# Performance work log

Measured on AMD Instinct MI355X. Metric: run time of the kernel, lower is better.

## Reference

```python
import jax, jax.numpy as jnp
import numpy as np

N = 50000
E = 400000
T = 7
FEAT = 7
H = 64
OUT = 4
LN_EPS = 1e-5


def _w(key, shape, scale=0.1):
    return jax.random.normal(key, shape, jnp.float32) * scale


def setup_inputs() -> dict:
    key = jax.random.key(0)
    ks = list(jax.random.split(key, 16))
    p = {}
    p['x'] = jax.random.normal(ks[0], (N, T, FEAT), jnp.float32)
    p['edge_index'] = jax.random.randint(ks[1], (2, E), 0, N)
    p['edge_weight'] = jax.random.uniform(ks[2], (E,), jnp.float32)
    p['Wg1'] = _w(ks[3], (FEAT, H)); p['bg1'] = jnp.zeros((H,), jnp.float32)
    p['Wg2'] = _w(ks[4], (H, H));    p['bg2'] = jnp.zeros((H,), jnp.float32)
    p['ln_g'] = jnp.ones((H,), jnp.float32); p['ln_b'] = jnp.zeros((H,), jnp.float32)
    p['Wih0'] = _w(ks[5], (4 * H, H)); p['Whh0'] = _w(ks[6], (4 * H, H))
    p['bih0'] = jnp.zeros((4 * H,), jnp.float32); p['bhh0'] = jnp.zeros((4 * H,), jnp.float32)
    p['Wih1'] = _w(ks[7], (4 * H, H)); p['Whh1'] = _w(ks[8], (4 * H, H))
    p['bih1'] = jnp.zeros((4 * H,), jnp.float32); p['bhh1'] = jnp.zeros((4 * H,), jnp.float32)
    p['Wm1'] = _w(ks[9], (H, H // 2));  p['bm1'] = jnp.zeros((H // 2,), jnp.float32)
    p['Wm2'] = _w(ks[10], (H // 2, OUT)); p['bm2'] = jnp.zeros((OUT,), jnp.float32)
    p['Wd1'] = _w(ks[11], (H, H // 4)); p['bd1'] = jnp.zeros((H // 4,), jnp.float32)
    p['Wd2'] = _w(ks[12], (H // 4, OUT)); p['bd2'] = jnp.zeros((OUT,), jnp.float32)
    return p


def gcn_norm(edge_index, edge_weight, n):
    # PyG GCNConv default: add self-loops (weight 1), symmetric normalization
    loop = jnp.arange(n)
    src = jnp.concatenate([edge_index[0], loop])
    dst = jnp.concatenate([edge_index[1], loop])
    w = jnp.concatenate([edge_weight, jnp.ones((n,), edge_weight.dtype)])
    deg = jax.ops.segment_sum(w, dst, num_segments=n)
    dinv = jnp.where(deg > 0, jax.lax.rsqrt(deg), 0.0)
    return src, dst, dinv[src] * w * dinv[dst]


def gcn(h, W, b, src, dst, norm, n):
    h = h @ W                          # [N, H] linear transform first
    m = h[src] * norm[:, None]         # gather + edge scaling  [E', H]
    return jax.ops.segment_sum(m, dst, num_segments=n) + b


def layer_norm(h, g, b):
    mu = jnp.mean(h, -1, keepdims=True)
    v = jnp.mean((h - mu) ** 2, -1, keepdims=True)
    return (h - mu) * jax.lax.rsqrt(v + LN_EPS) * g + b


def lstm_layer(xs, Wih, Whh, bih, bhh):
    # xs: [N, T, H]; torch gate order i, f, g, o
    n = xs.shape[0]
    h0 = jnp.zeros((n, Whh.shape[1]), xs.dtype)
    def step(carry, xt):
        h, c = carry
        gates = xt @ Wih.T + h @ Whh.T + bih + bhh
        i, f, g, o = jnp.split(gates, 4, axis=-1)
        c = jax.nn.sigmoid(f) * c + jax.nn.sigmoid(i) * jnp.tanh(g)
        h = jax.nn.sigmoid(o) * jnp.tanh(c)
        return (h, c), h
    _, hs = jax.lax.scan(step, (h0, h0), jnp.swapaxes(xs, 0, 1))
    return jnp.swapaxes(hs, 0, 1)


def reference(x, edge_index, edge_weight, Wg1, bg1, Wg2, bg2, ln_g, ln_b,
              Wih0, Whh0, bih0, bhh0, Wih1, Whh1, bih1, bhh1,
              Wm1, bm1, Wm2, bm2, Wd1, bd1, Wd2, bd2):
    n = x.shape[0]
    src, dst, norm = gcn_norm(edge_index, edge_weight, n)
    outs = []
    for t in range(x.shape[1]):  # fixed small T=7 (lookback)
        h = gcn(x[:, t, :], Wg1, bg1, src, dst, norm, n)
        h = jax.nn.leaky_relu(h, 0.01)
        # dropout is identity in eval mode
        h = gcn(h, Wg2, bg2, src, dst, norm, n)
        h = jax.nn.leaky_relu(h, 0.01)
        h = layer_norm(h, ln_g, ln_b)
        outs.append(h)
    seq = jnp.stack(outs, axis=1)  # [N, T, H]
    seq = lstm_layer(seq, Wih0, Whh0, bih0, bhh0)
    seq = lstm_layer(seq, Wih1, Whh1, bih1, bhh1)
    f = seq[:, -1, :]
    magnitude = jax.nn.relu(jax.nn.leaky_relu(f @ Wm1 + bm1, 0.01) @ Wm2 + bm2) + 1e-4
    direction = jax.nn.relu(f @ Wd1 + bd1) @ Wd2 + bd2
    return (magnitude, direction)
```

## Files before the change

### kernel.cpp

```cpp
#include <hip/hip_runtime.h>
#include <stdint.h>

#define NN 50000
#define NP 50048
#define EE 400000
#define TT 7
#define LN_EPS 1e-5f
#define SIG_SC (-1.4426950408889634f)
#define TANH_SC (2.8853900817779268f)

typedef __attribute__((ext_vector_type(8))) short bf16x8;
typedef __attribute__((ext_vector_type(4))) float f32x4;

__device__ __forceinline__ float leaky01(float x){ return x > 0.f ? x : 0.01f*x; }
__device__ __forceinline__ float fastrcp(float x){ return __builtin_amdgcn_rcpf(x); }
__device__ __forceinline__ float exp2fast(float x){ return __builtin_amdgcn_exp2f(x); }
__device__ __forceinline__ float sigmoidf(float x){ return fastrcp(1.f+__expf(-x)); }
__device__ __forceinline__ float tanhfast(float x){ return 1.f - 2.f*fastrcp(__expf(2.f*x)+1.f); }
__device__ __forceinline__ unsigned bf16rne(float f){
  unsigned u = __float_as_uint(f);
  return (u + 0x7fffu + ((u>>16)&1u)) >> 16;
}
__device__ __forceinline__ float bfu(unsigned u){ return __uint_as_float(u<<16); }
__device__ __forceinline__ float bfhi(unsigned u){ return __uint_as_float(u & 0xffff0000u); }

__global__ __launch_bounds__(256) void k_prep_all(
    const float* __restrict__ Wih0, const float* __restrict__ Whh0,
    const float* __restrict__ Wih1, const float* __restrict__ Whh1,
    const float* __restrict__ Wg2,
    const float* __restrict__ bih0, const float* __restrict__ bhh0,
    const float* __restrict__ bih1, const float* __restrict__ bhh1,
    const float* __restrict__ x,
    uint4* __restrict__ WF, uint4* __restrict__ WG2F, float* __restrict__ BS,
    ushort* __restrict__ xb, float* __restrict__ deg, int* __restrict__ counts){
  int b = blockIdx.x, tid = threadIdx.x;
  if (b < 32){
    int idx = b*256 + tid;
    int L = idx >> 12;
    int r = idx & 4095;
    int lane = r & 63;
    int e = r >> 6;
    int which = e & 1;
    int cs = e >> 1;
    int s = cs & 1, ct = cs >> 1;
    int row = ct*16 + (lane & 15);
    float sc = ((row >> 6) == 2) ? TANH_SC : SIG_SC;
    int kb = s*32 + (lane >> 4)*8;
    const float* W = L ? (which ? Whh1 : Wih1) : (which ? Whh0 : Wih0);
    const float* p = W + row*64 + kb;
    uint4 v;
    v.x = bf16rne(sc*p[0]) | (bf16rne(sc*p[1])<<16);
    v.y = bf16rne(sc*p[2]) | (bf16rne(sc*p[3])<<16);
    v.z = bf16rne(sc*p[4]) | (bf16rne(sc*p[5])<<16);
    v.w = bf16rne(sc*p[6]) | (bf16rne(sc*p[7])<<16);
    WF[idx] = v;
  } else if (b < 34){
    int idx = (b-32)*256 + tid;
    int lane = idx & 63, e = idx >> 6;
    int s = e & 1, ct = e >> 1;
    int kb = s*32 + (lane>>4)*8;
    int c = ct*16 + (lane&15);
    uint4 v;
    v.x = bf16rne(Wg2[(kb+0)*64+c]) | (bf16rne(Wg2[(kb+1)*64+c])<<16);
    v.y = bf16rne(Wg2[(kb+2)*64+c]) | (bf16rne(Wg2[(kb+3)*64+c])<<16);
    v.z = bf16rne(Wg2[(kb+4)*64+c]) | (bf16rne(Wg2[(kb+5)*64+c])<<16);
    v.w = bf16rne(Wg2[(kb+6)*64+c]) | (bf16rne(Wg2[(kb+7)*64+c])<<16);
    WG2F[idx] = v;
  } else if (b < 36){
    int L = b - 34;
    float sc = ((tid >> 6) == 2) ? TANH_SC : SIG_SC;
    BS[L*256+tid] = sc * (L ? (bih1[tid]+bhh1[tid]) : (bih0[tid]+bhh0[tid]));
  } else if (b < 232){
    int i = (b-36)*256 + tid;
    if (i < NN){ deg[i] = 1.0f; counts[i] = 0; }
  } else {
    int i = (b-232)*256 + tid;
    if (i < NN*49) xb[i] = (ushort)bf16rne(x[i]);
  }
}

__global__ void k_edge_count(const int* __restrict__ src, const int* __restrict__ dst,
                             const float* __restrict__ ew, float* deg, int* counts){
  int e = blockIdx.x*blockDim.x + threadIdx.x;
  if (e < EE){
    int d = dst[e];
    atomicAdd(&deg[d], ew[e]);
    atomicAdd(&counts[d], 1);
  }
}
__global__ __launch_bounds__(256) void k_scan_blk(const int* __restrict__ counts,
                                                  int* locincl, int* bsum, float* deg){
  int tid = threadIdx.x; int i = blockIdx.x*256 + tid;
  if (i < NN) deg[i] = rsqrtf(deg[i]);
  int v = (i < NN) ? counts[i] : 0;
  int lane = tid & 63;
  int val = v;
  #pragma unroll
  for (int off = 1; off < 64; off <<= 1){
    int u = __shfl_up(val, off, 64);
    if (lane >= off) val += u;
  }
  __shared__ int wsum[4];
  if (lane == 63) wsum[tid>>6] = val;
  __syncthreads();
  int w = tid >> 6, pre = 0;
  #pragma unroll
  for (int k = 0; k < 4; ++k) if (k < w) pre += wsum[k];
  int incl = val + pre;
  if (i < NN) locincl[i] = incl;
  if (tid == 255) bsum[blockIdx.x] = incl;
}
__global__ __launch_bounds__(256) void k_scan_top(const int* __restrict__ bsum, int* boff){
  int tid = threadIdx.x;
  int v = (tid < 196) ? bsum[tid] : 0;
  int lane = tid & 63;
  int val = v;
  #pragma unroll
  for (int off = 1; off < 64; off <<= 1){
    int u = __shfl_up(val, off, 64);
    if (lane >= off) val += u;
  }
  __shared__ int wsum[4];
  if (lane == 63) wsum[tid>>6] = val;
  __syncthreads();
  int w = tid >> 6, pre = 0;
  #pragma unroll
  for (int k = 0; k < 4; ++k) if (k < w) pre += wsum[k];
  if (tid < 196) boff[tid] = val + pre - v;
}
__global__ __launch_bounds__(256) void k_scan_fix(const int* __restrict__ locincl,
        const int* __restrict__ boff, const int* __restrict__ counts,
        int* rowptr, int* cursor){
  int i = blockIdx.x*256 + threadIdx.x;
  if (i < NN){
    int r = locincl[i] + boff[blockIdx.x];
    rowptr[i+1] = r;
    cursor[i] = r - counts[i];
  }
  if (i == 0) rowptr[0] = 0;
}
__global__ void k_scatter(const int* __restrict__ src, const int* __restrict__ dst,
                          const float* __restrict__ ew, const float* __restrict__ dinv,
                          int* cursor, uint2* e2){
  int e = blockIdx.x*blockDim.x + threadIdx.x;
  if (e < EE){
    int s = src[e], d = dst[e];
    float nv = dinv[s]*ew[e]*dinv[d];
    int slot = atomicAdd(&cursor[d], 1);
    e2[slot] = make_uint2((uint)s, __float_as_uint(nv));
  }
}

__global__ __launch_bounds__(256) void k_agg_x(const ushort* __restrict__ xb,
        const float* __restrict__ dinv, const int* __restrict__ rowptr,
        const uint2* __restrict__ e2, float* __restrict__ AX){
  int lane = threadIdx.x & 63, w = threadIdx.x >> 6;
  int i = blockIdx.x*4 + w;
  int beg = rowptr[i], end = rowptr[i+1];
  float di = dinv[i];
  float acc = 0.f;
  if (lane < 49) acc = di*di*bfu(xb[(size_t)i*49 + lane]);
  for (int s = beg; s < end; ++s){
    uint2 e = e2[s];
    int cs = (int)e.x; float wv = __uint_as_float(e.y);
    if (lane < 49) acc += wv * bfu(xb[(size_t)cs*49 + lane]);
  }
  if (lane < 49) AX[(size_t)i*49 + lane] = acc;
}
__global__ __launch_bounds__(256) void k_gcn2_mfma(const float* __restrict__ AX,
        const float* __restrict__ Wg1, const float* __restrict__ bg1,
        const uint4* __restrict__ WG2F, ushort* __restrict__ Z2p){
  __shared__ float sw1[448];
  __shared__ float sb1[64];
  __shared__ float sax[8*56];
  __shared__ __align__(16) ushort srb[64*68];
  int tid = threadIdx.x;
  int lane = tid & 63, w = tid >> 6;
  bf16x8 bw[4][2];
  #pragma unroll
  for (int ct = 0; ct < 4; ++ct)
    #pragma unroll
    for (int s = 0; s < 2; ++s){
      uint4 v = WG2F[(ct*2+s)*64 + lane];
      bw[ct][s] = *(bf16x8*)&v;
    }
  for (int i = tid; i < 448; i += 256) sw1[i] = Wg1[i];
  if (tid < 64) sb1[tid] = bg1[tid];
  int nbase = blockIdx.x*8;
  for (int i = tid; i < 448; i += 256){
    int n = i/56, c = i%56;
    sax[i] = (c < 49) ? AX[(size_t)(nbase+n)*49 + c] : 0.f;
  }
  __syncthreads();
  {
    int node = lane >> 3, t = lane & 7;
    float a[7];
    #pragma unroll
    for (int kk = 0; kk < 7; ++kk) a[kk] = sax[node*56 + t*7 + kk];
    ushort hv[16];
    #pragma unroll
    for (int j = 0; j < 16; ++j){
      int k = w*16 + j;
      float acc = sb1[k];
      #pragma unroll
      for (int kk = 0; kk < 7; ++kk) acc += a[kk]*sw1[kk*64+k];
      hv[j] = (ushort)bf16rne(leaky01(acc));
    }
    uint2* dst = (uint2*)&srb[lane*68 + w*16];
    #pragma unroll
    for (int q = 0; q < 4; ++q){
      uint2 v;
      v.x = (uint)hv[q*4+0] | ((uint)hv[q*4+1]<<16);
      v.y = (uint)hv[q*4+2] | ((uint)hv[q*4+3]<<16);
      dst[q] = v;
    }
  }
  __syncthreads();
  int col = lane & 15, quad = lane >> 4;
  bf16x8 afr[2];
  #pragma unroll
  for (int s = 0; s < 2; ++s){
    const ushort* pr = &srb[(w*16 + col)*68 + s*32 + quad*8];
    uint2 lo = *(const uint2*)pr;
    uint2 hi = *(const uint2*)(pr + 4);
    union { uint u[4]; bf16x8 b; } cv;
    cv.u[0]=lo.x; cv.u[1]=lo.y; cv.u[2]=hi.x; cv.u[3]=hi.y;
    afr[s] = cv.b;
  }
  f32x4 acc[4];
  #pragma unroll
  for (int ct = 0; ct < 4; ++ct) acc[ct] = (f32x4){0.f,0.f,0.f,0.f};
  #pragma unroll
  for (int ct = 0; ct < 4; ++ct)
    #pragma unroll
    for (int s = 0; s < 2; ++s)
      acc[ct] = __builtin_amdgcn_mfma_f32_16x16x32_bf16(afr[s], bw[ct][s], acc[ct], 0,0,0);
  int node = nbase + w*2 + (quad>>1);
  #pragma unroll
  for (int ct = 0; ct < 4; ++ct){
    uint2 v;
    v.x = bf16rne(acc[ct][0]) | (bf16rne(acc[ct][1])<<16);
    v.y = bf16rne(acc[ct][2]) | (bf16rne(acc[ct][3])<<16);
    size_t o = ((size_t)node*64 + ct*16 + col)*8 + (quad&1)*4;
    *(uint2*)(Z2p + o) = v;
  }
}
__global__ __launch_bounds__(256) void k_agg_ln_all(const ushort* __restrict__ Z2p,
        const float* __restrict__ dinv, const int* __restrict__ rowptr,
        const uint2* __restrict__ e2,
        const float* __restrict__ bg2, const float* __restrict__ lng,
        const float* __restrict__ lnb, ushort* __restrict__ XT){
  int lane = threadIdx.x & 63, w = threadIdx.x >> 6;
  int i = blockIdx.x*4 + w;
  int beg = rowptr[i], end = rowptr[i+1];
  float di = dinv[i];
  float swt = di*di;
  const uint4* zp = (const uint4*)Z2p;
  float acc[7];
  {
    uint4 v = zp[(size_t)i*64 + lane];
    acc[0] = swt*bfu(v.x); acc[1] = swt*bfhi(v.x);
    acc[2] = swt*bfu(v.y); acc[3] = swt*bfhi(v.y);
    acc[4] = swt*bfu(v.z); acc[5] = swt*bfhi(v.z);
    acc[6] = swt*bfu(v.w);
  }
  for (int s = beg; s < end; ++s){
    uint2 e = e2[s];
    int cs = (int)e.x; float wv = __uint_as_float(e.y);
    uint4 v = zp[(size_t)cs*64 + lane];
    acc[0] = fmaf(wv, bfu(v.x),  acc[0]);
    acc[1] = fmaf(wv, bfhi(v.x), acc[1]);
    acc[2] = fmaf(wv, bfu(v.y),  acc[2]);
    acc[3] = fmaf(wv, bfhi(v.y), acc[3]);
    acc[4] = fmaf(wv, bfu(v.z),  acc[4]);
    acc[5] = fmaf(wv, bfhi(v.z), acc[5]);
    acc[6] = fmaf(wv, bfu(v.w),  acc[6]);
  }
  float b2 = bg2[lane], gl = lng[lane], bl = lnb[lane];
  #pragma unroll
  for (int t = 0; t < 7; ++t){
    float a = leaky01(acc[t] + b2);
    float sum = a;
    #pragma unroll
    for (int off = 32; off >= 1; off >>= 1) sum += __shfl_xor(sum, off, 64);
    float mu = sum * (1.f/64.f);
    float d = a - mu;
    float vs = d*d;
    #pragma unroll
    for (int off = 32; off >= 1; off >>= 1) vs += __shfl_xor(vs, off, 64);
    float rs = rsqrtf(vs*(1.f/64.f) + LN_EPS);
    XT[(size_t)t*NP*64 + (size_t)i*64 + lane] = (ushort)bf16rne(d*rs*gl + bl);
  }
}

__global__ __launch_bounds__(256) void k_lstm_both(const ushort* __restrict__ xin,
        ushort* __restrict__ h1out, const uint4* __restrict__ WF,
        const float* __restrict__ BS){
  __shared__ __align__(16) ushort XL[7][16][72];
  int tid = threadIdx.x;
  int lane = tid & 63, cp = tid >> 6;
  int base = blockIdx.x*16;
  int col = lane & 15, quad = lane >> 4;
  for (int L = 0; L < 2; ++L){
    bf16x8 bwi[4][2], bwh[4][2];
    const uint4* wf = WF + L*4096;
    #pragma unroll
    for (int g = 0; g < 4; ++g){
      int ct = cp + 4*g;
      #pragma unroll
      for (int s = 0; s < 2; ++s){
        uint4 wi = wf[((ct*2+s)*2+0)*64 + lane];
        uint4 wh = wf[((ct*2+s)*2+1)*64 + lane];
        bwi[g][s] = *(bf16x8*)&wi;
        bwh[g][s] = *(bf16x8*)&wh;
      }
    }
    float bias[4];
    #pragma unroll
    for (int g = 0; g < 4; ++g) bias[g] = BS[L*256 + (cp + 4*g)*16 + col];
    f32x4 cst = (f32x4){0.f,0.f,0.f,0.f};
    bf16x8 hfr[2];
    hfr[0] = (bf16x8){0,0,0,0,0,0,0,0};
    hfr[1] = (bf16x8){0,0,0,0,0,0,0,0};

    for (int t = 0; t < 7; ++t){
      bf16x8 ax[2];
      if (L == 0){
        #pragma unroll
        for (int s = 0; s < 2; ++s)
          ax[s] = *(const bf16x8*)(xin + (size_t)t*NP*64
                          + (size_t)(base + col)*64 + s*32 + quad*8);
      } else {
        #pragma unroll
        for (int s = 0; s < 2; ++s)
          ax[s] = *(const bf16x8*)&XL[t][col][s*32 + quad*8];
      }
      f32x4 acc[4];
      #pragma unroll
      for (int g = 0; g < 4; ++g){
        float b = bias[g];
        acc[g] = (f32x4){b,b,b,b};
      }
      #pragma unroll
      for (int g = 0; g < 4; ++g){
        #pragma unroll
        for (int s = 0; s < 2; ++s){
          acc[g] = __builtin_amdgcn_mfma_f32_16x16x32_bf16(ax[s], bwi[g][s], acc[g], 0,0,0);
          acc[g] = __builtin_amdgcn_mfma_f32_16x16x32_bf16(hfr[s], bwh[g][s], acc[g], 0,0,0);
        }
      }
      __syncthreads();
      #pragma unroll
      for (int r = 0; r < 4; ++r){
        float ig = fastrcp(1.f + exp2fast(acc[0][r]));
        float fg = fastrcp(1.f + exp2fast(acc[1][r]));
        float gg = fmaf(-2.f, fastrcp(1.f + exp2fast(acc[2][r])), 1.f);
        float og = fastrcp(1.f + exp2fast(acc[3][r]));
        float cn = fmaf(fg, cst[r], ig*gg);
        cst[r] = cn;
        float tc = fmaf(-2.f, fastrcp(1.f + exp2fast(TANH_SC*cn)), 1.f);
        XL[t][quad*4 + r][cp*16 + col] = (ushort)bf16rne(og*tc);
      }
      __syncthreads();
      hfr[0] = *(const bf16x8*)&XL[t][col][quad*8];
      hfr[1] = *(const bf16x8*)&XL[t][col][32 + quad*8];
    }
  }
  if (tid < 128){
    int n2 = tid >> 3, off = (tid & 7)*8;
    uint4 v = *(const uint4*)&XL[6][n2][off];
    *(uint4*)(h1out + (size_t)(base+n2)*64 + off) = v;
  }
}

__global__ __launch_bounds__(256) void k_heads(const ushort* __restrict__ f,
        const float* __restrict__ Wm1, const float* __restrict__ bm1,
        const float* __restrict__ Wm2, const float* __restrict__ bm2,
        const float* __restrict__ Wd1, const float* __restrict__ bd1,
        const float* __restrict__ Wd2, const float* __restrict__ bd2,
        float* __restrict__ out){
  __shared__ float swm1[64*32];
  __shared__ float swm2[32*4];
  __shared__ float swd1[64*16];
  __shared__ float swd2[16*4];
  __shared__ float sbm1[32], sbm2[4], sbd1[16], sbd2[4];
  int tid = threadIdx.x;
  for (int i = tid; i < 2048; i += 256) swm1[i] = Wm1[i];
  for (int i = tid; i < 1024; i += 256) swd1[i] = Wd1[i];
  if (tid < 128) swm2[tid] = Wm2[tid];
  if (tid < 64) swd2[tid] = Wd2[tid];
  if (tid < 32) sbm1[tid] = bm1[tid];
  if (tid < 16) sbd1[tid] = bd1[tid];
  if (tid < 4){ sbm2[tid] = bm2[tid]; sbd2[tid] = bd2[tid]; }
  __syncthreads();
  int n = blockIdx.x*256 + tid;
  if (n >= NN) return;
  float fr[64];
  const uint* f2 = (const uint*)(f + (size_t)n*64);
  #pragma unroll
  for (int i = 0; i < 32; ++i){ uint u = f2[i]; fr[2*i] = bfu(u); fr[2*i+1] = bfhi(u); }
  float m1[32];
  #pragma unroll
  for (int c2 = 0; c2 < 32; ++c2) m1[c2] = sbm1[c2];
  for (int k = 0; k < 64; ++k){
    float fv = fr[k];
    #pragma unroll
    for (int c2 = 0; c2 < 32; ++c2) m1[c2] += fv*swm1[k*32+c2];
  }
  #pragma unroll
  for (int c2 = 0; c2 < 32; ++c2) m1[c2] = leaky01(m1[c2]);
  float mo[4];
  #pragma unroll
  for (int o = 0; o < 4; ++o) mo[o] = sbm2[o];
  for (int c2 = 0; c2 < 32; ++c2){
    float mv = m1[c2];
    #pragma unroll
    for (int o = 0; o < 4; ++o) mo[o] += mv*swm2[c2*4+o];
  }
  float d1[16];
  #pragma unroll
  for (int c2 = 0; c2 < 16; ++c2) d1[c2] = sbd1[c2];
  for (int k = 0; k < 64; ++k){
    float fv = fr[k];
    #pragma unroll
    for (int c2 = 0; c2 < 16; ++c2) d1[c2] += fv*swd1[k*16+c2];
  }
  #pragma unroll
  for (int c2 = 0; c2 < 16; ++c2) d1[c2] = fmaxf(d1[c2], 0.f);
  float dv[4];
  #pragma unroll
  for (int o = 0; o < 4; ++o) dv[o] = sbd2[o];
  for (int c2 = 0; c2 < 16; ++c2){
    float xv = d1[c2];
    #pragma unroll
    for (int o = 0; o < 4; ++o) dv[o] += xv*swd2[c2*4+o];
  }
  float4* o4 = (float4*)out;
  o4[n] = make_float4(fmaxf(mo[0],0.f)+1e-4f, fmaxf(mo[1],0.f)+1e-4f,
                      fmaxf(mo[2],0.f)+1e-4f, fmaxf(mo[3],0.f)+1e-4f);
  o4[NN + n] = make_float4(dv[0], dv[1], dv[2], dv[3]);
}

extern "C" void kernel_launch(void* const* d_in, const int* in_sizes, int n_in,
                              void* d_out, int out_size, void* d_ws, size_t ws_size,
                              hipStream_t stream){
  const float* x    = (const float*)d_in[0];
  const int*   eidx = (const int*)d_in[1];
  const float* ew   = (const float*)d_in[2];
  const float* Wg1  = (const float*)d_in[3];
  const float* bg1  = (const float*)d_in[4];
  const float* Wg2  = (const float*)d_in[5];
  const float* bg2  = (const float*)d_in[6];
  const float* lng  = (const float*)d_in[7];
  const float* lnb  = (const float*)d_in[8];
  const float* Wih0 = (const float*)d_in[9];
  const float* Whh0 = (const float*)d_in[10];
  const float* bih0 = (const float*)d_in[11];
  const float* bhh0 = (const float*)d_in[12];
  const float* Wih1 = (const float*)d_in[13];
  const float* Whh1 = (const float*)d_in[14];
  const float* bih1 = (const float*)d_in[15];
  const float* bhh1 = (const float*)d_in[16];
  const float* Wm1  = (const float*)d_in[17];
  const float* bm1  = (const float*)d_in[18];
  const float* Wm2  = (const float*)d_in[19];
  const float* bm2  = (const float*)d_in[20];
  const float* Wd1  = (const float*)d_in[21];
  const float* bd1  = (const float*)d_in[22];
  const float* Wd2  = (const float*)d_in[23];
  const float* bd2  = (const float*)d_in[24];
  const int* src = eidx;
  const int* dst = eidx + EE;
  float* out = (float*)d_out;

  char* p = (char*)d_ws;
  auto alloc = [&](size_t bytes)->char*{ char* r = p; p += (bytes + 255) & ~(size_t)255; return r; };
  float*  deg     = (float*)alloc((size_t)NN*4);
  int*    counts  = (int*)  alloc((size_t)NN*4);
  int*    rowptr  = (int*)  alloc((size_t)(NN+1)*4);
  int*    cursor  = (int*)  alloc((size_t)NN*4);
  int*    locincl = (int*)  alloc((size_t)NN*4);
  int*    bsum    = (int*)  alloc((size_t)256*4);
  int*    boff    = (int*)  alloc((size_t)256*4);
  uint2*  e2      = (uint2*)alloc((size_t)EE*8);
  uint4*  WF      = (uint4*)alloc((size_t)2*4096*16);
  uint4*  WG2F    = (uint4*)alloc((size_t)512*16);
  float*  BS      = (float*)alloc((size_t)2*256*4);
  ushort* xb      = (ushort*)alloc((size_t)NN*49*2);
  ushort* h1b     = (ushort*)alloc((size_t)NP*64*2);
  ushort* XT      = (ushort*)alloc((size_t)TT*NP*64*2);
  float*  AX      = (float*)alloc((size_t)NN*49*4);
  ushort* Z2p     = (ushort*)alloc((size_t)NN*64*8*2);

  int xblocks = (NN*49 + 255)/256;
  k_prep_all<<<232 + xblocks, 256, 0, stream>>>(Wih0, Whh0, Wih1, Whh1, Wg2,
      bih0, bhh0, bih1, bhh1, x, WF, WG2F, BS, xb, deg, counts);
  k_edge_count<<<(EE+255)/256, 256, 0, stream>>>(src, dst, ew, deg, counts);
  k_scan_blk<<<196, 256, 0, stream>>>(counts, locincl, bsum, deg);
  k_scan_top<<<1, 256, 0, stream>>>(bsum, boff);
  k_scan_fix<<<196, 256, 0, stream>>>(locincl, boff, counts, rowptr, cursor);
  k_scatter<<<(EE+255)/256, 256, 0, stream>>>(src, dst, ew, deg, cursor, e2);
  k_agg_x<<<NN/4, 256, 0, stream>>>(xb, deg, rowptr, e2, AX);
  k_gcn2_mfma<<<NN/8, 256, 0, stream>>>(AX, Wg1, bg1, WG2F, Z2p);
  k_agg_ln_all<<<NN/4, 256, 0, stream>>>(Z2p, deg, rowptr, e2, bg2, lng, lnb, XT);
  k_lstm_both<<<NP/16, 256, 0, stream>>>(XT, h1b, WF, BS);
  k_heads<<<(NN+255)/256, 256, 0, stream>>>(h1b, Wm1, bm1, Wm2, bm2, Wd1, bd1, Wd2, bd2, out);
}
```

Baseline: 408.8 us.

## Fuse output MLP heads into the LSTM kernel epilogue

Merges the separate heads kernel into the LSTM kernel: after the second LSTM layer, each block computes both MLP heads for its 16 nodes directly from the final hidden state in shared memory, spreading the work over 16 threads per node. This removes one launch and the global round trip of the final hidden state, and replaces a register-heavy one-thread-per-node heads kernel. It also drops the barrier before the gate write-back in layer 0. In exchange each LSTM block reloads all head weights into shared memory and uses more shared memory, which could lower occupancy.

```diff
diff --git a/kernel.cpp b/kernel.cpp
--- a/kernel.cpp
+++ b/kernel.cpp
@@ -15,8 +15,6 @@
 __device__ __forceinline__ float leaky01(float x){ return x > 0.f ? x : 0.01f*x; }
 __device__ __forceinline__ float fastrcp(float x){ return __builtin_amdgcn_rcpf(x); }
 __device__ __forceinline__ float exp2fast(float x){ return __builtin_amdgcn_exp2f(x); }
-__device__ __forceinline__ float sigmoidf(float x){ return fastrcp(1.f+__expf(-x)); }
-__device__ __forceinline__ float tanhfast(float x){ return 1.f - 2.f*fastrcp(__expf(2.f*x)+1.f); }
 __device__ __forceinline__ unsigned bf16rne(float f){
   unsigned u = __float_as_uint(f);
   return (u + 0x7fffu + ((u>>16)&1u)) >> 16;
@@ -293,14 +291,33 @@
   }
 }
 
-__global__ __launch_bounds__(256) void k_lstm_both(const ushort* __restrict__ xin,
-        ushort* __restrict__ h1out, const uint4* __restrict__ WF,
-        const float* __restrict__ BS){
+__global__ __launch_bounds__(256) void k_lstm_heads(const ushort* __restrict__ xin,
+        const uint4* __restrict__ WF, const float* __restrict__ BS,
+        const float* __restrict__ Wm1, const float* __restrict__ bm1,
+        const float* __restrict__ Wm2, const float* __restrict__ bm2,
+        const float* __restrict__ Wd1, const float* __restrict__ bd1,
+        const float* __restrict__ Wd2, const float* __restrict__ bd2,
+        float* __restrict__ out){
   __shared__ __align__(16) ushort XL[7][16][72];
+  __shared__ float swm1[2048];
+  __shared__ float swd1[1024];
+  __shared__ float swm2[128];
+  __shared__ float swd2[64];
+  __shared__ float sbm1[32], sbd1[16], sbm2[4], sbd2[4];
+  __shared__ float sm1[16][33];
+  __shared__ float sd1[16][17];
   int tid = threadIdx.x;
   int lane = tid & 63, cp = tid >> 6;
   int base = blockIdx.x*16;
   int col = lane & 15, quad = lane >> 4;
+  for (int i = tid; i < 2048; i += 256) swm1[i] = Wm1[i];
+  for (int i = tid; i < 1024; i += 256) swd1[i] = Wd1[i];
+  if (tid < 128) swm2[tid] = Wm2[tid];
+  if (tid < 64) swd2[tid] = Wd2[tid];
+  if (tid < 32) sbm1[tid] = bm1[tid];
+  if (tid < 16) sbd1[tid] = bd1[tid];
+  if (tid < 4){ sbm2[tid] = bm2[tid]; sbd2[tid] = bd2[tid]; }
+
   for (int L = 0; L < 2; ++L){
     bf16x8 bwi[4][2], bwh[4][2];
     const uint4* wf = WF + L*4096;
@@ -349,7 +366,7 @@
           acc[g] = __builtin_amdgcn_mfma_f32_16x16x32_bf16(hfr[s], bwh[g][s], acc[g], 0,0,0);
         }
       }
-      __syncthreads();
+      if (L) __syncthreads();
       #pragma unroll
       for (int r = 0; r < 4; ++r){
         float ig = fastrcp(1.f + exp2fast(acc[0][r]));
@@ -366,79 +383,30 @@
       hfr[1] = *(const bf16x8*)&XL[t][col][32 + quad*8];
     }
   }
-  if (tid < 128){
-    int n2 = tid >> 3, off = (tid & 7)*8;
-    uint4 v = *(const uint4*)&XL[6][n2][off];
-    *(uint4*)(h1out + (size_t)(base+n2)*64 + off) = v;
-  }
-}
-
-__global__ __launch_bounds__(256) void k_heads(const ushort* __restrict__ f,
-        const float* __restrict__ Wm1, const float* __restrict__ bm1,
-        const float* __restrict__ Wm2, const float* __restrict__ bm2,
-        const float* __restrict__ Wd1, const float* __restrict__ bd1,
-        const float* __restrict__ Wd2, const float* __restrict__ bd2,
-        float* __restrict__ out){
-  __shared__ float swm1[64*32];
-  __shared__ float swm2[32*4];
-  __shared__ float swd1[64*16];
-  __shared__ float swd2[16*4];
-  __shared__ float sbm1[32], sbm2[4], sbd1[16], sbd2[4];
-  int tid = threadIdx.x;
-  for (int i = tid; i < 2048; i += 256) swm1[i] = Wm1[i];
-  for (int i = tid; i < 1024; i += 256) swd1[i] = Wd1[i];
-  if (tid < 128) swm2[tid] = Wm2[tid];
-  if (tid < 64) swd2[tid] = Wd2[tid];
-  if (tid < 32) sbm1[tid] = bm1[tid];
-  if (tid < 16) sbd1[tid] = bd1[tid];
-  if (tid < 4){ sbm2[tid] = bm2[tid]; sbd2[tid] = bd2[tid]; }
+  int node = tid >> 4, sub = tid & 15;
+  int gn = base + node;
+  float m1a = sbm1[sub], m1b = sbm1[sub+16], d1v = sbd1[sub];
+  #pragma unroll 8
+  for (int k = 0; k < 64; ++k){
+    float fv = bfu(XL[6][node][k]);
+    m1a = fmaf(fv, swm1[k*32 + sub], m1a);
+    m1b = fmaf(fv, swm1[k*32 + sub + 16], m1b);
+    d1v = fmaf(fv, swd1[k*16 + sub], d1v);
+  }
+  sm1[node][sub] = leaky01(m1a);
+  sm1[node][sub+16] = leaky01(m1b);
+  sd1[node][sub] = fmaxf(d1v, 0.f);
   __syncthreads();
-  int n = blockIdx.x*256 + tid;
-  if (n >= NN) return;
-  float fr[64];
-  const uint* f2 = (const uint*)(f + (size_t)n*64);
-  #pragma unroll
-  for (int i = 0; i < 32; ++i){ uint u = f2[i]; fr[2*i] = bfu(u); fr[2*i+1] = bfhi(u); }
-  float m1[32];
-  #pragma unroll
-  for (int c2 = 0; c2 < 32; ++c2) m1[c2] = sbm1[c2];
-  for (int k = 0; k < 64; ++k){
-    float fv = fr[k];
-    #pragma unroll
-    for (int c2 = 0; c2 < 32; ++c2) m1[c2] += fv*swm1[k*32+c2];
-  }
-  #pragma unroll
-  for (int c2 = 0; c2 < 32; ++c2) m1[c2] = leaky01(m1[c2]);
-  float mo[4];
-  #pragma unroll
-  for (int o = 0; o < 4; ++o) mo[o] = sbm2[o];
-  for (int c2 = 0; c2 < 32; ++c2){
-    float mv = m1[c2];
-    #pragma unroll
-    for (int o = 0; o < 4; ++o) mo[o] += mv*swm2[c2*4+o];
-  }
-  float d1[16];
-  #pragma unroll
-  for (int c2 = 0; c2 < 16; ++c2) d1[c2] = sbd1[c2];
-  for (int k = 0; k < 64; ++k){
-    float fv = fr[k];
-    #pragma unroll
-    for (int c2 = 0; c2 < 16; ++c2) d1[c2] += fv*swd1[k*16+c2];
-  }
-  #pragma unroll
-  for (int c2 = 0; c2 < 16; ++c2) d1[c2] = fmaxf(d1[c2], 0.f);
-  float dv[4];
-  #pragma unroll
-  for (int o = 0; o < 4; ++o) dv[o] = sbd2[o];
-  for (int c2 = 0; c2 < 16; ++c2){
-    float xv = d1[c2];
-    #pragma unroll
-    for (int o = 0; o < 4; ++o) dv[o] += xv*swd2[c2*4+o];
-  }
-  float4* o4 = (float4*)out;
-  o4[n] = make_float4(fmaxf(mo[0],0.f)+1e-4f, fmaxf(mo[1],0.f)+1e-4f,
-                      fmaxf(mo[2],0.f)+1e-4f, fmaxf(mo[3],0.f)+1e-4f);
-  o4[NN + n] = make_float4(dv[0], dv[1], dv[2], dv[3]);
+  if (sub < 4 && gn < NN){
+    float mo = sbm2[sub];
+    #pragma unroll 8
+    for (int c = 0; c < 32; ++c) mo = fmaf(sm1[node][c], swm2[c*4+sub], mo);
+    float dv = sbd2[sub];
+    #pragma unroll 8
+    for (int c = 0; c < 16; ++c) dv = fmaf(sd1[node][c], swd2[c*4+sub], dv);
+    out[(size_t)gn*4 + sub] = fmaxf(mo, 0.f) + 1e-4f;
+    out[(size_t)NN*4 + (size_t)gn*4 + sub] = dv;
+  }
 }
 
 extern "C" void kernel_launch(void* const* d_in, const int* in_sizes, int n_in,
@@ -487,7 +455,6 @@
   uint4*  WG2F    = (uint4*)alloc((size_t)512*16);
   float*  BS      = (float*)alloc((size_t)2*256*4);
   ushort* xb      = (ushort*)alloc((size_t)NN*49*2);
-  ushort* h1b     = (ushort*)alloc((size_t)NP*64*2);
   ushort* XT      = (ushort*)alloc((size_t)TT*NP*64*2);
   float*  AX      = (float*)alloc((size_t)NN*49*4);
   ushort* Z2p     = (ushort*)alloc((size_t)NN*64*8*2);
@@ -503,6 +470,6 @@
   k_agg_x<<<NN/4, 256, 0, stream>>>(xb, deg, rowptr, e2, AX);
   k_gcn2_mfma<<<NN/8, 256, 0, stream>>>(AX, Wg1, bg1, WG2F, Z2p);
   k_agg_ln_all<<<NN/4, 256, 0, stream>>>(Z2p, deg, rowptr, e2, bg2, lng, lnb, XT);
-  k_lstm_both<<<NP/16, 256, 0, stream>>>(XT, h1b, WF, BS);
-  k_heads<<<(NN+255)/256, 256, 0, stream>>>(h1b, Wm1, bm1, Wm2, bm2, Wd1, bd1, Wd2, bd2, out);
-}
+  k_lstm_heads<<<NP/16, 256, 0, stream>>>(XT, WF, BS,
+      Wm1, bm1, Wm2, bm2, Wd1, bd1, Wd2, bd2, out);
+}
```

Result: no change. 405.3 us (-0.8%).
